# Kernel optimization log

Measured on AMD Instinct MI355X. Metric: run time of the kernel, lower is better.

## Reference

```python
import jax, jax.numpy as jnp
import numpy as np

N = 100000        # nodes
E = 1600000       # edges (avg degree 16)
IN_DIM = 128
OUT_DIM = 64
HEADS = 4
SLOPE = 0.2
CLIP_LO, CLIP_HI = 0.005, 10.0


def setup_inputs() -> dict:
    key = jax.random.key(0)
    k1, k2, k3, k4 = jax.random.split(key, 4)
    h = jax.random.normal(k1, (N, IN_DIM), dtype=jnp.float32)
    edges = jax.random.randint(k2, (2, E), 0, N, dtype=jnp.int64)
    # per-head Linear(in_dim, out_dim, bias=False) weights, applied as h @ W[k]
    W = jax.random.normal(k3, (HEADS, IN_DIM, OUT_DIM), dtype=jnp.float32) / np.sqrt(IN_DIM)
    # per-head Linear(2*out_dim, 1, bias=False) attention vectors
    a = jax.random.normal(k4, (HEADS, 2 * OUT_DIM), dtype=jnp.float32) / np.sqrt(2 * OUT_DIM)
    return {"h": h, "edges": edges, "W": W, "a": a}


def reference(h, edges, W, a):
    src, dst = edges[0], edges[1]
    outs = []
    for k in range(HEADS):  # small fixed loop over structurally distinct heads
        hw = h @ W[k]                                   # [N, OUT]
        # a(concat(hw[src], hw[dst])) == (hw @ a1)[src] + (hw @ a2)[dst]
        s_src = hw @ a[k, :OUT_DIM]                     # [N]
        s_dst = hw @ a[k, OUT_DIM:]                     # [N]
        logit = s_src[src] + s_dst[dst]                 # [E]
        e = jnp.clip(jnp.exp(jax.nn.leaky_relu(logit, SLOPE)), CLIP_LO, CLIP_HI)
        denom = jax.ops.segment_sum(e, dst, num_segments=N)   # per-dst softmax denom
        alpha = e / denom[dst]                          # [E]
        msg = hw[src] * alpha[:, None]                  # [E, OUT]
        outs.append(jax.ops.segment_sum(msg, dst, num_segments=N))
    # concatenate=False -> mean over heads
    return jnp.stack(outs, axis=-1).mean(axis=-1)
```

## Files before the change

### kernel.cpp

```cpp
#include <hip/hip_runtime.h>
#include <hip/hip_fp16.h>

#define N_NODES 100000
#define N_EDGES 1600000
#define IN_DIM  128
#define OUT_DIM 64
#define HEADS   4
#define SLOPE   0.2f
#define CLIP_LO 0.005f
#define CLIP_HI 10.0f
#define NRANGE 8
#define RANGE_SZ 12500
#define EDGES_PER_BLK 2048
#define CHUNKS 782
#define GEMM_BLOCKS 1563
#define S_BLOCKS 391
#define SCAT_BLOCKS (NRANGE * CHUNKS)
#define BUCKET 48
#define BIN_CAP 512

typedef short bf16x8 __attribute__((ext_vector_type(8)));
typedef float f32x4  __attribute__((ext_vector_type(4)));

__device__ __forceinline__ short f2bf(float x) {
    union { float f; unsigned u; } v; v.f = x;
    unsigned r = (v.u + 0x7FFF + ((v.u >> 16) & 1)) >> 16;
    return (short)r;
}
__device__ __forceinline__ unsigned short f2hbits(float x) {
    union { __half h; unsigned short u; } c; c.h = __float2half(x); return c.u;
}
__device__ __forceinline__ float hbits2f(unsigned short b) {
    union { __half h; unsigned short u; } c; c.u = b; return __half2float(c.h);
}

__global__ __launch_bounds__(256) void prep_kernel(const float* __restrict__ W,
                                                   const float* __restrict__ a,
                                                   short* __restrict__ WcatT,
                                                   float* __restrict__ Wa) {
    int idx = blockIdx.x * 256 + threadIdx.x;
    if (idx < 256 * 128) {
        int n = idx >> 7, i = idx & 127;
        int k = n >> 6, j = n & 63;
        WcatT[idx] = f2bf(W[((size_t)k * IN_DIM + i) * OUT_DIM + j]);
    } else if (idx < 256 * 128 + 1024) {
        int o = idx - 256 * 128;
        int k = o >> 8, half = (o >> 7) & 1, i = o & 127;
        const float* wrow = W + ((size_t)k * IN_DIM + i) * OUT_DIM;
        const float* av   = a + k * 2 * OUT_DIM + half * OUT_DIM;
        float acc = 0.f;
#pragma unroll 8
        for (int j = 0; j < OUT_DIM; ++j) acc += wrow[j] * av[j];
        Wa[o] = acc;
    }
}

__global__ __launch_bounds__(256) void s_bin(const float* __restrict__ h,
                                             const float* __restrict__ Wa,
                                             const int* __restrict__ edges,
                                             unsigned* __restrict__ bins,
                                             int* __restrict__ binCnt,
                                             float* __restrict__ sS,
                                             float* __restrict__ sD) {
    __shared__ __align__(16) char smem[16448];
    if (blockIdx.x >= S_BLOCKS) {
        int* bcnt = (int*)smem;
        unsigned (*bents)[BIN_CAP] = (unsigned(*)[BIN_CAP])(smem + 64);
        const int c = blockIdx.x - S_BLOCKS;
        const int base = c * EDGES_PER_BLK + threadIdx.x * 8;
        if (threadIdx.x < 8) bcnt[threadIdx.x] = 0;
        __syncthreads();
        if (base < N_EDGES) {
            int4 s0 = *(const int4*)(edges + base);
            int4 s1 = *(const int4*)(edges + base + 4);
            int4 d0 = *(const int4*)(edges + N_EDGES + base);
            int4 d1 = *(const int4*)(edges + N_EDGES + base + 4);
            int ss[8] = {s0.x, s0.y, s0.z, s0.w, s1.x, s1.y, s1.z, s1.w};
            int dd[8] = {d0.x, d0.y, d0.z, d0.w, d1.x, d1.y, d1.z, d1.w};
#pragma unroll
            for (int u = 0; u < 8; ++u) {
                unsigned d = (unsigned)dd[u];
                unsigned r = d / (unsigned)RANGE_SZ;
                int pos = atomicAdd(&bcnt[r], 1);
                if (pos < BIN_CAP)
                    bents[r][pos] = ((unsigned)ss[u] << 14) | (d - r * RANGE_SZ);
            }
        }
        __syncthreads();
#pragma unroll
        for (int r = 0; r < NRANGE; ++r) {
            int n = bcnt[r]; if (n > BIN_CAP) n = BIN_CAP;
            unsigned* gout = bins + ((size_t)r * CHUNKS + c) * BIN_CAP;
            for (int e = threadIdx.x; e < n; e += 256) gout[e] = bents[r][e];
            if (threadIdx.x == 0) binCnt[r * CHUNKS + c] = n;
        }
        return;
    }

    float* wa_s = (float*)smem;
    for (int t = threadIdx.x; t < HEADS * 2 * IN_DIM; t += 256) wa_s[t] = Wa[t];
    __syncthreads();
    int n = blockIdx.x * 256 + threadIdx.x;
    if (n >= N_NODES) return;
    const float4* hv = (const float4*)(h + (size_t)n * IN_DIM);
    const float4* wv = (const float4*)wa_s;
    float acc[8] = {0.f,0.f,0.f,0.f,0.f,0.f,0.f,0.f};
    for (int i4 = 0; i4 < IN_DIM / 4; ++i4) {
        float4 hx = hv[i4];
#pragma unroll
        for (int k2 = 0; k2 < 8; ++k2) {
            float4 w = wv[k2 * (IN_DIM / 4) + i4];
            acc[k2] += hx.x * w.x + hx.y * w.y + hx.z * w.z + hx.w * w.w;
        }
    }
    *(float4*)(sS + (size_t)n * 4) = make_float4(acc[0], acc[2], acc[4], acc[6]);
    *(float4*)(sD + (size_t)n * 4) = make_float4(acc[1], acc[3], acc[5], acc[7]);
}

__device__ __forceinline__ float edge_e(float x) {
    x = x > 0.f ? x : SLOPE * x;
    float ev = __expf(x);
    return fminf(fmaxf(ev, CLIP_LO), CLIP_HI);
}

__global__ __launch_bounds__(256) void gemm_scatter(const float* __restrict__ h,
                                                    const short* __restrict__ WcatT,
                                                    const unsigned* __restrict__ bins,
                                                    const int* __restrict__ binCnt,
                                                    const float4* __restrict__ sArrS,
                                                    const float4* __restrict__ sArrD,
                                                    int* __restrict__ cnt,
                                                    uint4* __restrict__ csr,
                                                    unsigned char* __restrict__ hw8,
                                                    float* __restrict__ scaleArr) {
    __shared__ __align__(16) short As[64][136];

    if (blockIdx.x < SCAT_BLOCKS) {
        const int r = blockIdx.x & (NRANGE - 1);
        const int c = blockIdx.x >> 3;
        int n = binCnt[r * CHUNKS + c];
        if (n > BIN_CAP) n = BIN_CAP;
        const unsigned* ge = bins + ((size_t)r * CHUNKS + c) * BIN_CAP;
        const int dbase = r * RANGE_SZ;

        const int e0 = threadIdx.x, e1 = threadIdx.x + 256;
        bool v0 = e0 < n, v1 = e1 < n;
        unsigned u0 = v0 ? ge[e0] : 0;
        unsigned u1 = v1 ? ge[e1] : 0;
        int s0 = u0 >> 14, d0 = dbase + (u0 & 16383);
        int s1 = u1 >> 14, d1 = dbase + (u1 & 16383);
        float4 sv0, dv0, sv1, dv1;
        if (v0) { sv0 = sArrS[s0]; dv0 = sArrD[d0]; }
        if (v1) { sv1 = sArrS[s1]; dv1 = sArrD[d1]; }

        if (v0) {
            uint4 rec;
            rec.x = (unsigned)s0;
            rec.y = f2hbits(edge_e(sv0.x + dv0.x)) | ((unsigned)f2hbits(edge_e(sv0.y + dv0.y)) << 16);
            rec.z = f2hbits(edge_e(sv0.z + dv0.z)) | ((unsigned)f2hbits(edge_e(sv0.w + dv0.w)) << 16);
            rec.w = 0;
            int pos = atomicAdd(&cnt[d0], 1);
            if (pos < BUCKET) csr[(size_t)d0 * BUCKET + pos] = rec;
        }
        if (v1) {
            uint4 rec;
            rec.x = (unsigned)s1;
            rec.y = f2hbits(edge_e(sv1.x + dv1.x)) | ((unsigned)f2hbits(edge_e(sv1.y + dv1.y)) << 16);
            rec.z = f2hbits(edge_e(sv1.z + dv1.z)) | ((unsigned)f2hbits(edge_e(sv1.w + dv1.w)) << 16);
            rec.w = 0;
            int pos = atomicAdd(&cnt[d1], 1);
            if (pos < BUCKET) csr[(size_t)d1 * BUCKET + pos] = rec;
        }
        return;
    }

    const int row0 = (blockIdx.x - SCAT_BLOCKS) * 64;
    const int tid  = threadIdx.x;

#pragma unroll
    for (int u = 0; u < 4; ++u) {
        int e = (tid + u * 256) * 8;
        int r = e >> 7, c = e & 127;
        int grow = row0 + r; if (grow >= N_NODES) grow = N_NODES - 1;
        const float* hp = h + (size_t)grow * IN_DIM + c;
        float4 v0 = *(const float4*)hp;
        float4 v1 = *(const float4*)(hp + 4);
        bf16x8 b;
        b[0]=f2bf(v0.x); b[1]=f2bf(v0.y); b[2]=f2bf(v0.z); b[3]=f2bf(v0.w);
        b[4]=f2bf(v1.x); b[5]=f2bf(v1.y); b[6]=f2bf(v1.z); b[7]=f2bf(v1.w);
        *(bf16x8*)&As[r][c] = b;
    }
    __syncthreads();

    const int wv = tid >> 6, lane = tid & 63;
    const int lrow = lane & 15;
    const int lk   = (lane >> 4) * 8;

    bf16x8 bfr[4][4];
#pragma unroll
    for (int nt = 0; nt < 4; ++nt)
#pragma unroll
        for (int ks = 0; ks < 4; ++ks)
            bfr[nt][ks] = *(const bf16x8*)(WcatT + (size_t)(wv * 64 + nt * 16 + lrow) * 128 + ks * 32 + lk);

    f32x4 acc[4][4] = {};
#pragma unroll
    for (int ks = 0; ks < 4; ++ks) {
        bf16x8 afr[4];
#pragma unroll
        for (int mt = 0; mt < 4; ++mt)
            afr[mt] = *(const bf16x8*)&As[mt * 16 + lrow][ks * 32 + lk];
#pragma unroll
        for (int mt = 0; mt < 4; ++mt)
#pragma unroll
            for (int nt = 0; nt < 4; ++nt)
                acc[mt][nt] = __builtin_amdgcn_mfma_f32_16x16x32_bf16(afr[mt], bfr[nt][ks], acc[mt][nt], 0, 0, 0);
    }

    const int rgrp = lane >> 4;
#pragma unroll
    for (int mt = 0; mt < 4; ++mt)
#pragma unroll
        for (int reg = 0; reg < 4; ++reg) {
            int g = row0 + mt * 16 + rgrp * 4 + reg;
            float m = fmaxf(fmaxf(fabsf(acc[mt][0][reg]), fabsf(acc[mt][1][reg])),
                            fmaxf(fabsf(acc[mt][2][reg]), fabsf(acc[mt][3][reg])));
#pragma unroll
            for (int off = 1; off < 16; off <<= 1)
                m = fmaxf(m, __shfl_xor(m, off));
            float scale = m > 0.f ? m * (1.f / 127.f) : 1.f;
            float inv   = m > 0.f ? 127.f / m : 0.f;
            uchar4 q;
            q.x = (unsigned char)(int)rintf(acc[mt][0][reg] * inv + 128.f);
            q.y = (unsigned char)(int)rintf(acc[mt][1][reg] * inv + 128.f);
            q.z = (unsigned char)(int)rintf(acc[mt][2][reg] * inv + 128.f);
            q.w = (unsigned char)(int)rintf(acc[mt][3][reg] * inv + 128.f);
            if (g < N_NODES) {
                *(uchar4*)(hw8 + (size_t)g * 256 + wv * 64 + lrow * 4) = q;
                if (lrow == 0) scaleArr[(size_t)g * 4 + wv] = scale;
            }
        }
}

__device__ __forceinline__ float pickw(const uint4& r, int kh) {
    unsigned wp = (kh & 2) ? r.z : r.y;
    return hbits2f((unsigned short)((kh & 1) ? (wp >> 16) : (wp & 0xffff)));
}
__device__ __forceinline__ void qacc(float4& lo, float4& hi, uint2 g, float ws) {
    float wb = -128.f * ws;
    unsigned x = g.x, y = g.y;
    lo.x += fmaf((float)( x        & 255u), ws, wb);
    lo.y += fmaf((float)((x >> 8 ) & 255u), ws, wb);
    lo.z += fmaf((float)((x >> 16) & 255u), ws, wb);
    lo.w += fmaf((float)( x >> 24        ), ws, wb);
    hi.x += fmaf((float)( y        & 255u), ws, wb);
    hi.y += fmaf((float)((y >> 8 ) & 255u), ws, wb);
    hi.z += fmaf((float)((y >> 16) & 255u), ws, wb);
    hi.w += fmaf((float)( y >> 24        ), ws, wb);
}

__global__ __launch_bounds__(256) void msg_csr(const int* __restrict__ cnt,
                                               const uint4* __restrict__ csr,
                                               const unsigned char* __restrict__ hw8,
                                               const float* __restrict__ scaleArr,
                                               float* __restrict__ out) {
    int wid  = (blockIdx.x * 256 + threadIdx.x) >> 6;
    int lane = threadIdx.x & 63;
    if (wid >= N_NODES) return;
    const size_t start = (size_t)wid * BUCKET;
    int dg = cnt[wid];
    if (dg > BUCKET) dg = BUCKET;

    const int es = lane >> 5;
    const int kh = (lane & 31) >> 3;
    const int cg = lane & 7;
    const size_t coff = (size_t)((kh << 6) + (cg << 3));

    float4 alo = make_float4(0.f,0.f,0.f,0.f), ahi = make_float4(0.f,0.f,0.f,0.f);
    float den = 0.f;
    int i = 0;
    for (; i + 8 <= dg; i += 8) {
        uint4 r0 = csr[start + i     + es];
        uint4 r1 = csr[start + i + 2 + es];
        uint4 r2 = csr[start + i + 4 + es];
        uint4 r3 = csr[start + i + 6 + es];
        uint2 g0 = *(const uint2*)(hw8 + (((size_t)r0.x) << 8) + coff);
        uint2 g1 = *(const uint2*)(hw8 + (((size_t)r1.x) << 8) + coff);
        uint2 g2 = *(const uint2*)(hw8 + (((size_t)r2.x) << 8) + coff);
        uint2 g3 = *(const uint2*)(hw8 + (((size_t)r3.x) << 8) + coff);
        float sc0 = scaleArr[(size_t)r0.x * 4 + kh];
        float sc1 = scaleArr[(size_t)r1.x * 4 + kh];
        float sc2 = scaleArr[(size_t)r2.x * 4 + kh];
        float sc3 = scaleArr[(size_t)r3.x * 4 + kh];
        float w0 = pickw(r0, kh);
        float w1 = pickw(r1, kh);
        float w2 = pickw(r2, kh);
        float w3 = pickw(r3, kh);
        den += (w0 + w1) + (w2 + w3);
        qacc(alo, ahi, g0, w0 * sc0);
        qacc(alo, ahi, g1, w1 * sc1);
        qacc(alo, ahi, g2, w2 * sc2);
        qacc(alo, ahi, g3, w3 * sc3);
    }
    for (; i + 4 <= dg; i += 4) {
        uint4 r0 = csr[start + i     + es];
        uint4 r1 = csr[start + i + 2 + es];
        uint2 g0 = *(const uint2*)(hw8 + (((size_t)r0.x) << 8) + coff);
        uint2 g1 = *(const uint2*)(hw8 + (((size_t)r1.x) << 8) + coff);
        float sc0 = scaleArr[(size_t)r0.x * 4 + kh];
        float sc1 = scaleArr[(size_t)r1.x * 4 + kh];
        float w0 = pickw(r0, kh);
        float w1 = pickw(r1, kh);
        den += w0 + w1;
        qacc(alo, ahi, g0, w0 * sc0);
        qacc(alo, ahi, g1, w1 * sc1);
    }
    for (; i < dg; i += 2) {
        int idx = i + es;
        bool valid = idx < dg;
        if (idx >= dg) idx = dg - 1;
        uint4 r = csr[start + idx];
        uint2 g = *(const uint2*)(hw8 + (((size_t)r.x) << 8) + coff);
        float sc = scaleArr[(size_t)r.x * 4 + kh];
        float w = valid ? pickw(r, kh) : 0.f;
        den += w;
        qacc(alo, ahi, g, w * sc);
    }

    den += __shfl_xor(den, 32);
    float invk = den > 0.f ? 0.25f / den : 0.f;
    alo.x *= invk; alo.y *= invk; alo.z *= invk; alo.w *= invk;
    ahi.x *= invk; ahi.y *= invk; ahi.z *= invk; ahi.w *= invk;

#pragma unroll
    for (int off = 8; off < 64; off <<= 1) {
        alo.x += __shfl_xor(alo.x, off); alo.y += __shfl_xor(alo.y, off);
        alo.z += __shfl_xor(alo.z, off); alo.w += __shfl_xor(alo.w, off);
        ahi.x += __shfl_xor(ahi.x, off); ahi.y += __shfl_xor(ahi.y, off);
        ahi.z += __shfl_xor(ahi.z, off); ahi.w += __shfl_xor(ahi.w, off);
    }
    if (lane < 8) {
        float* op = out + (size_t)wid * OUT_DIM + (cg << 1);
        *(float2*)(op)      = make_float2(alo.x, ahi.x);
        *(float2*)(op + 16) = make_float2(alo.y, ahi.y);
        *(float2*)(op + 32) = make_float2(alo.z, ahi.z);
        *(float2*)(op + 48) = make_float2(alo.w, ahi.w);
    }
}

extern "C" void kernel_launch(void* const* d_in, const int* in_sizes, int n_in,
                              void* d_out, int out_size, void* d_ws, size_t ws_size,
                              hipStream_t stream) {
    const float* h     = (const float*)d_in[0];
    const int*   edges = (const int*)d_in[1];
    const float* W     = (const float*)d_in[2];
    const float* a     = (const float*)d_in[3];
    float* out = (float*)d_out;

    char* ws = (char*)d_ws;
    unsigned char* hw8      = (unsigned char*)(ws);
    float*  scaleArr= (float*) (ws + 25600000);
    float*  sArrS   = (float*) (ws + 27200000);
    float*  sArrD   = (float*) (ws + 28800000);
    short*  WcatT   = (short*) (ws + 30400000);
    float*  Wa      = (float*) (ws + 30465536);
    int*    cnt     = (int*)   (ws + 30469632);
    int*    binCnt  = (int*)   (ws + 30869632);
    uint4*  csr     = (uint4*) (ws + 30894720);

    unsigned* bins = (unsigned*)d_out;

    hipMemsetAsync(cnt, 0, (size_t)N_NODES * sizeof(int), stream);

    prep_kernel<<<132, 256, 0, stream>>>(W, a, WcatT, Wa);
    s_bin<<<S_BLOCKS + CHUNKS, 256, 0, stream>>>(h, Wa, edges, bins, binCnt,
                                                 sArrS, sArrD);
    gemm_scatter<<<SCAT_BLOCKS + GEMM_BLOCKS, 256, 0, stream>>>(
        h, WcatT, bins, binCnt, (const float4*)sArrS, (const float4*)sArrD,
        cnt, csr, hw8, scaleArr);

    msg_csr<<<(N_NODES + 3) / 4, 256, 0, stream>>>(cnt, csr, hw8, scaleArr, out);
}
```

Measured before the change: 207.3 us.

## Bin edges into fine destination ranges and count per range in LDS

Edges are now binned into 250 destination ranges of 400 nodes each instead of 8 ranges of 12500. One block per range builds the bucketed CSR, using shared-memory counters and a shared-memory copy of the destination scores in place of global atomics. This removes the separate memset of the global count array and the contention of global atomics. The cost is far fewer scatter blocks, each walking many mostly empty 32-entry bin slots, which risks a long tail next to the GEMM blocks. The fixed bin cap of 32 could also drop edges if a chunk puts more than 32 edges into one range.

```diff
diff --git a/kernel.cpp b/kernel.cpp
--- a/kernel.cpp
+++ b/kernel.cpp
@@ -9,15 +9,14 @@
 #define SLOPE   0.2f
 #define CLIP_LO 0.005f
 #define CLIP_HI 10.0f
-#define NRANGE 8
-#define RANGE_SZ 12500
+#define NRANGE 250
+#define RANGE_SZ 400
 #define EDGES_PER_BLK 2048
 #define CHUNKS 782
 #define GEMM_BLOCKS 1563
 #define S_BLOCKS 391
-#define SCAT_BLOCKS (NRANGE * CHUNKS)
 #define BUCKET 48
-#define BIN_CAP 512
+#define BIN_CAP 32
 
 typedef short bf16x8 __attribute__((ext_vector_type(8)));
 typedef float f32x4  __attribute__((ext_vector_type(4)));
@@ -62,13 +61,13 @@
                                              int* __restrict__ binCnt,
                                              float* __restrict__ sS,
                                              float* __restrict__ sD) {
-    __shared__ __align__(16) char smem[16448];
+    __shared__ __align__(16) char smem[33024];
     if (blockIdx.x >= S_BLOCKS) {
         int* bcnt = (int*)smem;
-        unsigned (*bents)[BIN_CAP] = (unsigned(*)[BIN_CAP])(smem + 64);
+        unsigned* bents = (unsigned*)(smem + 1024);
         const int c = blockIdx.x - S_BLOCKS;
         const int base = c * EDGES_PER_BLK + threadIdx.x * 8;
-        if (threadIdx.x < 8) bcnt[threadIdx.x] = 0;
+        for (int t = threadIdx.x; t < NRANGE; t += 256) bcnt[t] = 0;
         __syncthreads();
         if (base < N_EDGES) {
             int4 s0 = *(const int4*)(edges + base);
@@ -83,16 +82,15 @@
                 unsigned r = d / (unsigned)RANGE_SZ;
                 int pos = atomicAdd(&bcnt[r], 1);
                 if (pos < BIN_CAP)
-                    bents[r][pos] = ((unsigned)ss[u] << 14) | (d - r * RANGE_SZ);
+                    bents[r * BIN_CAP + pos] = ((unsigned)ss[u] << 9) | (d - r * RANGE_SZ);
             }
         }
         __syncthreads();
-#pragma unroll
-        for (int r = 0; r < NRANGE; ++r) {
+        for (int idx = threadIdx.x; idx < NRANGE * BIN_CAP; idx += 256) {
+            int r = idx >> 5, i = idx & 31;
             int n = bcnt[r]; if (n > BIN_CAP) n = BIN_CAP;
-            unsigned* gout = bins + ((size_t)r * CHUNKS + c) * BIN_CAP;
-            for (int e = threadIdx.x; e < n; e += 256) gout[e] = bents[r][e];
-            if (threadIdx.x == 0) binCnt[r * CHUNKS + c] = n;
+            if (i < n) bins[((size_t)r * CHUNKS + c) * BIN_CAP + i] = bents[r * BIN_CAP + i];
+            if (i == 0) binCnt[r * CHUNKS + c] = n;
         }
         return;
     }
@@ -133,48 +131,48 @@
                                                     uint4* __restrict__ csr,
                                                     unsigned char* __restrict__ hw8,
                                                     float* __restrict__ scaleArr) {
-    __shared__ __align__(16) short As[64][136];
-
-    if (blockIdx.x < SCAT_BLOCKS) {
-        const int r = blockIdx.x & (NRANGE - 1);
-        const int c = blockIdx.x >> 3;
-        int n = binCnt[r * CHUNKS + c];
-        if (n > BIN_CAP) n = BIN_CAP;
-        const unsigned* ge = bins + ((size_t)r * CHUNKS + c) * BIN_CAP;
-        const int dbase = r * RANGE_SZ;
-
-        const int e0 = threadIdx.x, e1 = threadIdx.x + 256;
-        bool v0 = e0 < n, v1 = e1 < n;
-        unsigned u0 = v0 ? ge[e0] : 0;
-        unsigned u1 = v1 ? ge[e1] : 0;
-        int s0 = u0 >> 14, d0 = dbase + (u0 & 16383);
-        int s1 = u1 >> 14, d1 = dbase + (u1 & 16383);
-        float4 sv0, dv0, sv1, dv1;
-        if (v0) { sv0 = sArrS[s0]; dv0 = sArrD[d0]; }
-        if (v1) { sv1 = sArrS[s1]; dv1 = sArrD[d1]; }
-
-        if (v0) {
+    __shared__ __align__(16) char smem[64 * 136 * 2];
+
+    if (blockIdx.x < NRANGE) {
+        int*    cntL = (int*)smem;
+        float4* dvL  = (float4*)(smem + 1664);
+        int*    bcL  = (int*)(smem + 8064);
+        const int r = blockIdx.x;
+        for (int t = threadIdx.x; t < RANGE_SZ; t += 256) {
+            cntL[t] = 0;
+            dvL[t]  = sArrD[r * RANGE_SZ + t];
+        }
+        for (int t = threadIdx.x; t < CHUNKS; t += 256) bcL[t] = binCnt[r * CHUNKS + t];
+        __syncthreads();
+
+        const int TOT = CHUNKS * BIN_CAP;
+        for (int slot = threadIdx.x; slot < TOT; slot += 256) {
+            int c = slot >> 5, i = slot & 31;
+            if (i >= bcL[c]) continue;
+            unsigned u = bins[((size_t)r * CHUNKS + c) * BIN_CAP + i];
+            int s  = u >> 9;
+            int dl = u & 511;
+            float4 sv = sArrS[s];
+            float4 dv = dvL[dl];
             uint4 rec;
-            rec.x = (unsigned)s0;
-            rec.y = f2hbits(edge_e(sv0.x + dv0.x)) | ((unsigned)f2hbits(edge_e(sv0.y + dv0.y)) << 16);
-            rec.z = f2hbits(edge_e(sv0.z + dv0.z)) | ((unsigned)f2hbits(edge_e(sv0.w + dv0.w)) << 16);
+            rec.x = (unsigned)s;
+            rec.y = f2hbits(edge_e(sv.x + dv.x)) | ((unsigned)f2hbits(edge_e(sv.y + dv.y)) << 16);
+            rec.z = f2hbits(edge_e(sv.z + dv.z)) | ((unsigned)f2hbits(edge_e(sv.w + dv.w)) << 16);
             rec.w = 0;
-            int pos = atomicAdd(&cnt[d0], 1);
-            if (pos < BUCKET) csr[(size_t)d0 * BUCKET + pos] = rec;
-        }
-        if (v1) {
-            uint4 rec;
-            rec.x = (unsigned)s1;
-            rec.y = f2hbits(edge_e(sv1.x + dv1.x)) | ((unsigned)f2hbits(edge_e(sv1.y + dv1.y)) << 16);
-            rec.z = f2hbits(edge_e(sv1.z + dv1.z)) | ((unsigned)f2hbits(edge_e(sv1.w + dv1.w)) << 16);
-            rec.w = 0;
-            int pos = atomicAdd(&cnt[d1], 1);
-            if (pos < BUCKET) csr[(size_t)d1 * BUCKET + pos] = rec;
+            int pos = atomicAdd(&cntL[dl], 1);
+            if (pos < BUCKET)
+                csr[(size_t)(r * RANGE_SZ + dl) * BUCKET + pos] = rec;
+        }
+        __syncthreads();
+        for (int t = threadIdx.x; t < RANGE_SZ; t += 256) {
+            int v = cntL[t];
+            cnt[r * RANGE_SZ + t] = v > BUCKET ? BUCKET : v;
         }
         return;
     }
 
-    const int row0 = (blockIdx.x - SCAT_BLOCKS) * 64;
+    short (*As)[136] = (short(*)[136])smem;
+    const int row0 = (blockIdx.x - NRANGE) * 64;
     const int tid  = threadIdx.x;
 
 #pragma unroll
@@ -358,7 +356,7 @@
     float* out = (float*)d_out;
 
     char* ws = (char*)d_ws;
-    unsigned char* hw8      = (unsigned char*)(ws);
+    unsigned char* hw8 = (unsigned char*)(ws);
     float*  scaleArr= (float*) (ws + 25600000);
     float*  sArrS   = (float*) (ws + 27200000);
     float*  sArrD   = (float*) (ws + 28800000);
@@ -366,16 +364,14 @@
     float*  Wa      = (float*) (ws + 30465536);
     int*    cnt     = (int*)   (ws + 30469632);
     int*    binCnt  = (int*)   (ws + 30869632);
-    uint4*  csr     = (uint4*) (ws + 30894720);
+    uint4*  csr     = (uint4*) (ws + 31651632);
 
     unsigned* bins = (unsigned*)d_out;
-
-    hipMemsetAsync(cnt, 0, (size_t)N_NODES * sizeof(int), stream);
 
     prep_kernel<<<132, 256, 0, stream>>>(W, a, WcatT, Wa);
     s_bin<<<S_BLOCKS + CHUNKS, 256, 0, stream>>>(h, Wa, edges, bins, binCnt,
                                                  sArrS, sArrD);
-    gemm_scatter<<<SCAT_BLOCKS + GEMM_BLOCKS, 256, 0, stream>>>(
+    gemm_scatter<<<NRANGE + GEMM_BLOCKS, 256, 0, stream>>>(
         h, WcatT, bins, binCnt, (const float4*)sArrS, (const float4*)sArrD,
         cnt, csr, hw8, scaleArr);
 
```

Measured after the change: 199.8 us. 1.04x faster.
